# Performance work log

Measured on AMD Instinct MI355X. Metric: run time of the kernel, lower is better.

## Reference

```python
import jax, jax.numpy as jnp
import numpy as np

N_NODES = 100000
N_EDGES = 1600000
IN_FEATS = 128
N_HIDDEN = 128
N_CLASSES = 16
INIT_EPS = 0.0
N_GIN_LAYERS = 4  # n_layers + 1


def setup_inputs() -> dict:
    key = jax.random.key(0)
    ks = jax.random.split(key, 16)
    features = jax.random.normal(ks[0], (N_NODES, IN_FEATS), dtype=jnp.float32)
    src = jax.random.randint(ks[1], (N_EDGES,), 0, N_NODES, dtype=jnp.int64)
    dst = jax.random.randint(ks[2], (N_EDGES,), 0, N_NODES, dtype=jnp.int64)
    def linear(k, fin, fout):
        bound = 1.0 / np.sqrt(fin)
        kw, kb = jax.random.split(k)
        W = jax.random.uniform(kw, (fin, fout), jnp.float32, -bound, bound)
        b = jax.random.uniform(kb, (fout,), jnp.float32, -bound, bound)
        return W, b
    W0, b0 = linear(ks[3], IN_FEATS, N_HIDDEN)
    W1, b1 = linear(ks[4], N_HIDDEN, N_HIDDEN)
    W2, b2 = linear(ks[5], N_HIDDEN, N_HIDDEN)
    W3, b3 = linear(ks[6], N_HIDDEN, N_CLASSES)
    eps = jnp.full((N_GIN_LAYERS,), INIT_EPS, dtype=jnp.float32)
    return {"features": features, "src": src, "dst": dst,
            "W0": W0, "b0": b0, "W1": W1, "b1": b1,
            "W2": W2, "b2": b2, "W3": W3, "b3": b3, "eps": eps}


def _mean_agg(h, src, dst, inv_deg):
    # gather neighbor features along edges, sum into dst, divide by in-degree
    agg = jax.ops.segment_sum(h[src], dst, num_segments=N_NODES)
    return agg * inv_deg


def _gin_layer(h, src, dst, inv_deg, eps, W, b, relu):
    z = (1.0 + eps) * h + _mean_agg(h, src, dst, inv_deg)
    out = z @ W + b  # Dropout is identity in eval mode
    return jax.nn.relu(out) if relu else out


def reference(features, src, dst, W0, b0, W1, b1, W2, b2, W3, b3, eps):
    deg = jax.ops.segment_sum(jnp.ones((src.shape[0],), features.dtype), dst,
                              num_segments=N_NODES)
    inv_deg = (1.0 / jnp.maximum(deg, 1.0))[:, None]
    h = _gin_layer(features, src, dst, inv_deg, eps[0], W0, b0, relu=True)
    h = _gin_layer(h, src, dst, inv_deg, eps[1], W1, b1, relu=True)
    h = _gin_layer(h, src, dst, inv_deg, eps[2], W2, b2, relu=True)
    h = _gin_layer(h, src, dst, inv_deg, eps[3], W3, b3, relu=False)
    return h
```

## Files before the change

kernel.cpp:

```cpp
#include <hip/hip_runtime.h>

#define NODES 100000
#define EDGES 1600000
#define FEATS 128
#define NCLS  16

#define BSH    6
#define BNODES 64
#define NB     ((NODES + BNODES - 1) / BNODES)
#define CHUNK  8192
#define NBLK   ((EDGES + CHUNK - 1) / CHUNK)
#define NHIST  (NB * NBLK)
#define BCAP   2048
#define NGRP   ((NODES + 15) / 16)

typedef unsigned int  u32;
typedef unsigned short u16;
typedef unsigned long long u64;
typedef __attribute__((ext_vector_type(8))) short short8;
typedef __attribute__((ext_vector_type(4))) float f32x4;

__device__ __forceinline__ float b2f(u16 v){ return __uint_as_float(((u32)v)<<16); }
__device__ __forceinline__ u16 f2b(float f){
  u32 u = __float_as_uint(f);
  u += 0x7fffu + ((u>>16)&1u);
  return (u16)(u>>16);
}
__device__ __forceinline__ float blo(u32 p){ return __uint_as_float(p<<16); }
__device__ __forceinline__ float bhi(u32 p){ return __uint_as_float(p & 0xffff0000u); }

__device__ __forceinline__ void gload16(const u16* g, u16* l){
  __builtin_amdgcn_global_load_lds(
      (const __attribute__((address_space(1))) u32*)g,
      (__attribute__((address_space(3))) u32*)l, 16, 0, 0);
}


__global__ __launch_bounds__(256) void pA_k(const int* __restrict__ dst,
                                            int* __restrict__ gh, int E){
  __shared__ int hist[NB];
  int t = threadIdx.x, blk = blockIdx.x;
  for (int j = t; j < NB; j += 256) hist[j] = 0;
  __syncthreads();
  int e0 = blk*CHUNK, e1 = e0 + CHUNK; if (e1 > E) e1 = E;
  for (int e = e0 + t; e < e1; e += 256) atomicAdd(&hist[dst[e] >> BSH], 1);
  __syncthreads();
  for (int j = t; j < NB; j += 256) gh[j*NBLK + blk] = hist[j];
}


__global__ __launch_bounds__(256) void scan1_k(const int* __restrict__ in, int* __restrict__ out,
                                               int* __restrict__ bsum, int n){
  __shared__ int sh[256];
  int t = threadIdx.x;
  int base = blockIdx.x*2048 + t*8;
  int v[8]; int s = 0;
  #pragma unroll
  for (int j=0;j<8;++j) v[j] = (base+j < n) ? in[base+j] : 0;
  #pragma unroll
  for (int j=0;j<8;++j){ int tmp = v[j]; v[j] = s; s += tmp; }
  sh[t] = s; __syncthreads();
  for (int off=1; off<256; off<<=1){
    int x = (t>=off) ? sh[t-off] : 0;
    __syncthreads();
    sh[t] += x;
    __syncthreads();
  }
  int excl = sh[t] - s;
  #pragma unroll
  for (int j=0;j<8;++j) if (base+j < n) out[base+j] = excl + v[j];
  if (t == 255) bsum[blockIdx.x] = sh[255];
}

__global__ __launch_bounds__(256) void scan2_k(const int* __restrict__ bsum,
                                               int* __restrict__ boff, int nb){
  __shared__ int sh[256];
  int t = threadIdx.x;
  int v = (t < nb) ? bsum[t] : 0;
  sh[t] = v; __syncthreads();
  for (int off=1; off<256; off<<=1){
    int x = (t>=off) ? sh[t-off] : 0;
    __syncthreads();
    sh[t] += x;
    __syncthreads();
  }
  if (t < nb) boff[t] = sh[t] - v;
}

__global__ void scan3_k(int* __restrict__ gscan, const int* __restrict__ boff,
                        int* __restrict__ bstart, int n){
  int i = blockIdx.x*256 + threadIdx.x;
  if (i < n){
    int v = gscan[i] + boff[i>>11];
    gscan[i] = v;
    if (i % NBLK == 0) bstart[i / NBLK] = v;
    if (i == 0) bstart[NB] = EDGES;
  }
}


__global__ __launch_bounds__(256) void pC_k(const int* __restrict__ src,
    const int* __restrict__ dst, const int* __restrict__ gscan,
    u32* __restrict__ elist, int E){
  __shared__ int A[NB];
  __shared__ int B[NB];
  __shared__ int sp[256];
  __shared__ u32 pay[CHUNK];
  __shared__ u16 bkt[CHUNK];
  int t = threadIdx.x, blk = blockIdx.x;
  for (int j = t; j < NB; j += 256) A[j] = 0;
  __syncthreads();
  int e0 = blk*CHUNK, e1 = e0 + CHUNK; if (e1 > E) e1 = E;
  int cnt = e1 - e0;
  for (int e = e0 + t; e < e1; e += 256) atomicAdd(&A[dst[e] >> BSH], 1);
  __syncthreads();
  {
    int base = t*7;
    int cv[7]; int s = 0;
    #pragma unroll
    for (int j=0;j<7;++j){ int idx = base+j; cv[j] = (idx < NB) ? A[idx] : 0; s += cv[j]; }
    sp[t] = s; __syncthreads();
    for (int off=1; off<256; off<<=1){
      int x = (t>=off) ? sp[t-off] : 0;
      __syncthreads();
      sp[t] += x;
      __syncthreads();
    }
    int run = sp[t] - s;
    #pragma unroll
    for (int j=0;j<7;++j){
      int idx = base+j;
      if (idx < NB){ A[idx] = run; B[idx] = run; run += cv[j]; }
    }
  }
  __syncthreads();
  for (int j = t; j < NB; j += 256) A[j] = gscan[j*NBLK + blk] - A[j];
  __syncthreads();
  for (int e = e0 + t; e < e1; e += 256){
    int d = dst[e];
    int b = d >> BSH;
    u32 w = ((u32)(d & (BNODES-1)) << 17) | (u32)src[e];
    int r = atomicAdd(&B[b], 1);
    pay[r] = w; bkt[r] = (u16)b;
  }
  __syncthreads();
  for (int i = t; i < cnt; i += 256){
    int b = bkt[i];
    elist[i + A[b]] = pay[i];
  }
}


__global__ __launch_bounds__(256) void csr_k(u32* __restrict__ elist,
    const int* __restrict__ bstart, int* __restrict__ offs, int* __restrict__ degs,
    float* __restrict__ invd, int M){
  __shared__ int hist[BNODES];
  __shared__ int pos[BNODES];
  __shared__ u32 buf[BCAP];
  __shared__ u32 buf2[BCAP];
  int b = blockIdx.x, t = threadIdx.x;
  if (b == 0 && t == 0) offs[M] = EDGES;
  if (t < BNODES) hist[t] = 0;
  __syncthreads();
  int s0 = bstart[b];
  int cnt = bstart[b+1] - s0; if (cnt > BCAP) cnt = BCAP;
  u32* el = elist + s0;
  for (int e = t; e < cnt; e += 256){
    u32 w = el[e];
    buf[e] = w;
    atomicAdd(&hist[w>>17], 1);
  }
  __syncthreads();
  if (t < BNODES){
    int v = hist[t];
    int s = v;
    for (int off = 1; off < BNODES; off <<= 1){
      int x = __shfl_up(s, off);
      if (t >= off) s += x;
    }
    int excl = s - v;
    pos[t] = excl;
    int node = b*BNODES + t;
    if (node < M){
      offs[node] = s0 + excl;
      degs[node] = v;
      invd[node] = 1.f / fmaxf((float)v, 1.f);
    }
  }
  __syncthreads();
  for (int e = t; e < cnt; e += 256){
    u32 w = buf[e];
    int p = atomicAdd(&pos[w>>17], 1);
    buf2[p] = w;
  }
  __syncthreads();
  for (int e = t; e < cnt; e += 256) el[e] = buf2[e];
}


__global__ __launch_bounds__(256) void convw4_k(const float* __restrict__ W0,
    const float* __restrict__ W1, const float* __restrict__ W2,
    const float* __restrict__ W3, u16* __restrict__ Wt0, u16* __restrict__ Wt1,
    u16* __restrict__ Wt2, u16* __restrict__ Wt3){
  int i = blockIdx.x*256 + threadIdx.x;
  if (i < 128*128){
    int k = i >> 7, n = i & 127;
    Wt0[n*128 + k] = f2b(W0[i]);
    Wt1[n*128 + k] = f2b(W1[i]);
    Wt2[n*128 + k] = f2b(W2[i]);
  }
  if (i < 128*16){
    int k = i >> 4, n = i & 15;
    Wt3[n*128 + k] = f2b(W3[i]);
  }
}


template<int NT, bool F32>
__global__ __launch_bounds__(256) void gemm_k(const void* __restrict__ hv,
                                              const u16* __restrict__ Wt,
                                              u16* __restrict__ y, int M){
  const int K = FEATS;
  const int N = NT*16;
  __shared__ __align__(128) u16 wbuf[NT*16*128];
  int t = threadIdx.x;
  #pragma unroll
  for (int i=0;i<NT;++i){
    int g16 = i*2048 + t*8;
    int n   = g16 >> 7;
    int cb2 = (g16 & 127) * 2;
    short8 wv = *(const short8*)(Wt + g16);
    *(short8*)((char*)wbuf + n*256 + (cb2 ^ ((n&7)<<4))) = wv;
  }
  __syncthreads();

  int lane = t & 63;
  int wave = t >> 6;
  int m    = lane & 15;
  int quad = lane >> 4;
  int row0 = (blockIdx.x*4 + wave)*16;
  if (row0 >= M) return;
  int rowA = row0 + m; if (rowA > M-1) rowA = M-1;

  f32x4 acc[NT];
  #pragma unroll
  for (int j=0;j<NT;++j) acc[j] = (f32x4){0.f,0.f,0.f,0.f};

  #pragma unroll
  for (int kb=0; kb<4; ++kb){
    short8 a;
    if constexpr (F32){
      const float* pa = (const float*)hv + (size_t)rowA*K + quad*8 + kb*32;
      float4 x0 = ((const float4*)pa)[0];
      float4 x1 = ((const float4*)pa)[1];
      union { u16 u[8]; short8 s; } au;
      au.u[0]=f2b(x0.x); au.u[1]=f2b(x0.y); au.u[2]=f2b(x0.z); au.u[3]=f2b(x0.w);
      au.u[4]=f2b(x1.x); au.u[5]=f2b(x1.y); au.u[6]=f2b(x1.z); au.u[7]=f2b(x1.w);
      a = au.s;
    } else {
      const u16* pa = (const u16*)hv + (size_t)rowA*K + quad*8 + kb*32;
      a = *(const short8*)pa;
    }
    #pragma unroll
    for (int j=0;j<NT;++j){
      short8 b = *(const short8*)((const char*)wbuf + (j*16+m)*256
                                  + ((kb*64 + quad*16) ^ ((m&7)<<4)));
      acc[j] = __builtin_amdgcn_mfma_f32_16x16x32_bf16(a, b, acc[j], 0, 0, 0);
    }
  }

  #pragma unroll
  for (int j=0;j<NT;++j){
    #pragma unroll
    for (int r=0;r<4;++r){
      int row = row0 + quad*4 + r;
      if (row < M) y[(size_t)row*N + j*16 + m] = f2b(acc[j][r]);
    }
  }
}


#define TRRD(dstv, lit) asm volatile("ds_read_b64_tr_b16 %0, %1 offset:" lit \
                                     : "=v"(dstv) : "v"(trb0))

template<int NTO>
__global__ __launch_bounds__(256) void fagg_k(const u16* __restrict__ y,
    const u32* __restrict__ el, const int* __restrict__ offs,
    const float* __restrict__ invd, const float* __restrict__ bias,
    const float* __restrict__ epsv, int ei,
    const u16* __restrict__ Wn,
    u16* __restrict__ yout){
  __shared__ __align__(128) u16 ybuf[4][4096];
  __shared__ __align__(128) u16 wbuf[NTO*16*128];
  int t = threadIdx.x;
  int lane = t & 63;
  int wave = t >> 6;
  int grp = blockIdx.x*4 + wave;
  bool valid = grp < NGRP;

  #pragma unroll
  for (int i=0;i<NTO;++i){
    int g16 = i*2048 + t*8;
    int n   = g16 >> 7;
    int cb2 = (g16 & 127) * 2;
    short8 wv = *(const short8*)(Wn + g16);
    *(short8*)((char*)wbuf + n*256 + (cb2 ^ ((n&7)<<4))) = wv;
  }
  __syncthreads();
  if (!valid) return;

  int v0 = grp << 4;
  int m    = lane & 15;
  int quad = lane >> 4;
  int li   = lane & 31;
  u32 tgt = (u32)(((grp & 3) << 4) + m);

  u16* lb0 = &ybuf[wave][0];
  typedef __attribute__((address_space(3))) u16 lds_u16;
  u32 lbaddr = (u32)(size_t)(lds_u16*)lb0;
  u32 trb0 = lbaddr + (u32)(quad*2048) + (u32)(m*8);

  int rsel = (lane & 7) >> 1;
  int gcol = ((lane >> 3) << 4) + ((lane & 1) << 3);

  int e0 = offs[v0];
  int e1 = offs[v0 + 16];
  int nstep = (e1 - e0 + 31) >> 5;

  f32x4 acc[8];
  #pragma unroll
  for (int cb=0;cb<8;++cb) acc[cb] = (f32x4){0.f,0.f,0.f,0.f};

  for (int st = 0; st < nstep; ++st){
    int idx = e0 + (st<<5) + li;
    u32 w = (idx < e1) ? el[idx] : 0xFFFE0000u;

    #pragma unroll
    for (int i=0;i<8;++i){
      u32 ws = (u32)__shfl((int)w, 4*i + rsel);
      int srow = (int)(ws & 0x1FFFFu);
      gload16(y + ((size_t)srow << 7) + gcol, lb0 + i*512);
    }

    union { u32 wv[4]; short8 s; } au;
    #pragma unroll
    for (int p=0;p<4;++p){
      u32 w0 = (u32)__shfl((int)w, quad*8 + 2*p);
      u32 w1 = (u32)__shfl((int)w, quad*8 + 2*p + 1);
      au.wv[p] = (((w0>>17) == tgt) ? 0x3F80u : 0u)
               | (((w1>>17) == tgt) ? 0x3F800000u : 0u);
    }

    asm volatile("s_waitcnt vmcnt(0)" ::: "memory");
    __builtin_amdgcn_sched_barrier(0);

    u64 tt[16];
    TRRD(tt[0],  "0");    TRRD(tt[1],  "1024");
    TRRD(tt[2],  "128");  TRRD(tt[3],  "1152");
    TRRD(tt[4],  "256");  TRRD(tt[5],  "1280");
    TRRD(tt[6],  "384");  TRRD(tt[7],  "1408");
    TRRD(tt[8],  "512");  TRRD(tt[9],  "1536");
    TRRD(tt[10], "640");  TRRD(tt[11], "1664");
    TRRD(tt[12], "768");  TRRD(tt[13], "1792");
    TRRD(tt[14], "896");  TRRD(tt[15], "1920");
    asm volatile("s_waitcnt lgkmcnt(0)" ::: "memory");
    __builtin_amdgcn_sched_barrier(0);

    #pragma unroll
    for (int cb=0;cb<8;++cb){
      union { u64 d[2]; short8 s; } bu;
      bu.d[0] = tt[2*cb]; bu.d[1] = tt[2*cb+1];
      acc[cb] = __builtin_amdgcn_mfma_f32_16x16x32_bf16(au.s, bu.s, acc[cb], 0, 0, 0);
    }
  }

  float myinv = invd[v0 + m];
  float invr[4];
  #pragma unroll
  for (int r=0;r<4;++r) invr[r] = __shfl(myinv, quad*4 + r);
  float e1s = 1.f + epsv[ei];
  u16* zl = lb0;
  #pragma unroll
  for (int cb=0;cb<8;++cb){
    float bi = bias[cb*16 + m];
    #pragma unroll
    for (int r=0;r<4;++r){
      size_t off = (size_t)(v0 + quad*4 + r)*FEATS + cb*16 + m;
      float self = b2f(y[off]);
      float h = fmaxf(e1s*self + invr[r]*acc[cb][r] + bi, 0.f);
      zl[(quad*4 + r)*136 + cb*16 + m] = f2b(h);
    }
  }

  short8 af[4];
  #pragma unroll
  for (int kb=0;kb<4;++kb)
    af[kb] = *(const short8*)(zl + m*136 + kb*32 + quad*8);

  #pragma unroll
  for (int nb=0;nb<NTO;++nb){
    f32x4 a2 = (f32x4){0.f,0.f,0.f,0.f};
    #pragma unroll
    for (int kb=0;kb<4;++kb){
      short8 bf = *(const short8*)((const char*)wbuf + (nb*16+m)*256
                                   + ((kb*64 + quad*16) ^ ((m&7)<<4)));
      a2 = __builtin_amdgcn_mfma_f32_16x16x32_bf16(af[kb], bf, a2, 0, 0, 0);
    }
    #pragma unroll
    for (int r=0;r<4;++r)
      yout[(size_t)(v0 + quad*4 + r)*(NTO*16) + nb*16 + m] = f2b(a2[r]);
  }
}


__global__ __launch_bounds__(256) void aggF2_k(const u16* __restrict__ y,
    const u32* __restrict__ el, const int* __restrict__ offs,
    const int* __restrict__ degs, const float* __restrict__ invd,
    const float* __restrict__ bias, const float* __restrict__ epsv,
    float* __restrict__ out, int M){
  int lane = threadIdx.x & 63;
  int v = blockIdx.x*4 + (threadIdx.x >> 6);
  if (v >= M) return;
  int sub = lane >> 3;
  int f2  = lane & 7;
  const u32* y2 = (const u32*)y;
  int start = offs[v], deg = degs[v];
  float acc0 = 0.f, acc1 = 0.f;
  for (int e = sub; e < deg; e += 8){
    u32 s = el[start + e] & 0x1FFFFu;
    u32 p = y2[(size_t)s*8 + f2];
    acc0 += blo(p); acc1 += bhi(p);
  }
  acc0 += __shfl_xor(acc0, 8);  acc1 += __shfl_xor(acc1, 8);
  acc0 += __shfl_xor(acc0, 16); acc1 += __shfl_xor(acc1, 16);
  acc0 += __shfl_xor(acc0, 32); acc1 += __shfl_xor(acc1, 32);
  if (sub == 0){
    u32 pv = y2[(size_t)v*8 + f2];
    float2 bi = ((const float2*)bias)[f2];
    float e1s = 1.f + epsv[3];
    float inv = invd[v];
    out[(size_t)v*NCLS + 2*f2    ] = e1s*blo(pv) + inv*acc0 + bi.x;
    out[(size_t)v*NCLS + 2*f2 + 1] = e1s*bhi(pv) + inv*acc1 + bi.y;
  }
}


extern "C" void kernel_launch(void* const* d_in, const int* in_sizes, int n_in,
                              void* d_out, int out_size, void* d_ws, size_t ws_size,
                              hipStream_t stream){
  const float* feats = (const float*)d_in[0];
  const int*   src   = (const int*)d_in[1];
  const int*   dst   = (const int*)d_in[2];
  const float* W0 = (const float*)d_in[3];  const float* b0 = (const float*)d_in[4];
  const float* W1 = (const float*)d_in[5];  const float* b1 = (const float*)d_in[6];
  const float* W2 = (const float*)d_in[7];  const float* b2 = (const float*)d_in[8];
  const float* W3 = (const float*)d_in[9];  const float* b3 = (const float*)d_in[10];
  const float* eps = (const float*)d_in[11];

  char* w = (char*)d_ws;
  auto alloc = [&](size_t bytes)->char*{
    char* p = w; w += (bytes + 255) & ~(size_t)255; return p;
  };
  int*  gh    = (int*)alloc(sizeof(int)*NHIST);
  int*  gscan = (int*)alloc(sizeof(int)*NHIST);
  int*  bsum  = (int*)alloc(sizeof(int)*256);
  int*  boff  = (int*)alloc(sizeof(int)*256);
  int*  bstart= (int*)alloc(sizeof(int)*(NB+1));
  int*  offs  = (int*)alloc(sizeof(int)*(NODES+1));
  int*  degs  = (int*)alloc(sizeof(int)*NODES);
  float* invd = (float*)alloc(sizeof(float)*NODES);
  u32*  elist = (u32*)alloc(sizeof(u32)*EDGES);
  u16*  hb    = (u16*)alloc(sizeof(u16)*(size_t)NODES*FEATS);
  u16*  yb    = (u16*)alloc(sizeof(u16)*(size_t)NODES*FEATS);
  u16*  Wt0   = (u16*)alloc(sizeof(u16)*128*128);
  u16*  Wt1   = (u16*)alloc(sizeof(u16)*128*128);
  u16*  Wt2   = (u16*)alloc(sizeof(u16)*128*128);
  u16*  Wt3   = (u16*)alloc(sizeof(u16)*16*128);

  pA_k<<<NBLK, 256, 0, stream>>>(dst, gh, EDGES);
  int snb = (NHIST + 2047)/2048;
  scan1_k<<<snb, 256, 0, stream>>>(gh, gscan, bsum, NHIST);
  scan2_k<<<1, 256, 0, stream>>>(bsum, boff, snb);
  scan3_k<<<(NHIST+255)/256, 256, 0, stream>>>(gscan, boff, bstart, NHIST);
  pC_k<<<NBLK, 256, 0, stream>>>(src, dst, gscan, elist, EDGES);
  csr_k<<<NB, 256, 0, stream>>>(elist, bstart, offs, degs, invd, NODES);

  convw4_k<<<(128*128+255)/256, 256, 0, stream>>>(W0, W1, W2, W3, Wt0, Wt1, Wt2, Wt3);

  int gblocks = (NODES + 63)/64;
  int mblocks = (NGRP + 3)/4;
  int ablocks = (NODES + 3)/4;

  gemm_k<8, true><<<gblocks, 256, 0, stream>>>(feats, Wt0, yb, NODES);
  fagg_k<8><<<mblocks, 256, 0, stream>>>(yb, elist, offs, invd, b0, eps, 0, Wt1, hb);
  fagg_k<8><<<mblocks, 256, 0, stream>>>(hb, elist, offs, invd, b1, eps, 1, Wt2, yb);
  fagg_k<1><<<mblocks, 256, 0, stream>>>(yb, elist, offs, invd, b2, eps, 2, Wt3, hb);
  aggF2_k<<<ablocks, 256, 0, stream>>>(hb, elist, offs, degs, invd, b3, eps, (float*)d_out, NODES);
}
```

Before: 412.5 us.

## Double-buffer neighbor gathers and process two node groups per wave in fused aggregation

The fused aggregate+GEMM kernel now gives each wave two 16-node groups, g and g+HNG, and runs their edge steps as one continuous loop. Edge-index loads are prefetched one step ahead, and row gathers go into a double-buffered LDS region, so the next step's global loads overlap the current step's transpose reads and MFMAs. The weight tile is no longer staged in LDS and is read directly from global memory in the per-group epilogue. This removes the block-wide weight preload and barrier, at the cost of uncached-in-LDS weight reads, hand-tuned vmcnt counts that must match the number of outstanding loads, and half as many waves to hide latency.

```diff
diff --git a/kernel.cpp b/kernel.cpp
--- a/kernel.cpp
+++ b/kernel.cpp
@@ -13,6 +13,7 @@
 #define NHIST  (NB * NBLK)
 #define BCAP   2048
 #define NGRP   ((NODES + 15) / 16)
+#define HNG    3125
 
 typedef unsigned int  u32;
 typedef unsigned short u16;
@@ -281,7 +282,7 @@
 
 
 #define TRRD(dstv, lit) asm volatile("ds_read_b64_tr_b16 %0, %1 offset:" lit \
-                                     : "=v"(dstv) : "v"(trb0))
+                                     : "=v"(dstv) : "v"(trb_i))
 
 template<int NTO>
 __global__ __launch_bounds__(256) void fagg_k(const u16* __restrict__ y,
@@ -290,32 +291,20 @@
     const float* __restrict__ epsv, int ei,
     const u16* __restrict__ Wn,
     u16* __restrict__ yout){
-  __shared__ __align__(128) u16 ybuf[4][4096];
-  __shared__ __align__(128) u16 wbuf[NTO*16*128];
+  __shared__ __align__(128) u16 ybuf[4][2][4096];
   int t = threadIdx.x;
   int lane = t & 63;
   int wave = t >> 6;
-  int grp = blockIdx.x*4 + wave;
-  bool valid = grp < NGRP;
-
-  #pragma unroll
-  for (int i=0;i<NTO;++i){
-    int g16 = i*2048 + t*8;
-    int n   = g16 >> 7;
-    int cb2 = (g16 & 127) * 2;
-    short8 wv = *(const short8*)(Wn + g16);
-    *(short8*)((char*)wbuf + n*256 + (cb2 ^ ((n&7)<<4))) = wv;
-  }
-  __syncthreads();
-  if (!valid) return;
-
-  int v0 = grp << 4;
+  int g0 = blockIdx.x*4 + wave;
+  if (g0 >= HNG) return;
+  int g1 = g0 + HNG;
   int m    = lane & 15;
   int quad = lane >> 4;
   int li   = lane & 31;
-  u32 tgt = (u32)(((grp & 3) << 4) + m);
-
-  u16* lb0 = &ybuf[wave][0];
+  u32 tgtA = (u32)(((g0 & 3) << 4) + m);
+  u32 tgtB = (u32)(((g1 & 3) << 4) + m);
+
+  u16* lb0 = &ybuf[wave][0][0];
   typedef __attribute__((address_space(3))) u16 lds_u16;
   u32 lbaddr = (u32)(size_t)(lds_u16*)lb0;
   u32 trb0 = lbaddr + (u32)(quad*2048) + (u32)(m*8);
@@ -323,37 +312,105 @@
   int rsel = (lane & 7) >> 1;
   int gcol = ((lane >> 3) << 4) + ((lane & 1) << 3);
 
-  int e0 = offs[v0];
-  int e1 = offs[v0 + 16];
-  int nstep = (e1 - e0 + 31) >> 5;
+  int e0A = offs[g0 << 4], e1A = offs[(g0 << 4) + 16];
+  int e0B = offs[g1 << 4], e1B = offs[(g1 << 4) + 16];
+  int SA = (e1A - e0A + 31) >> 5; if (SA < 1) SA = 1;
+  int SB = (e1B - e0B + 31) >> 5; if (SB < 1) SB = 1;
+  int S  = SA + SB;
 
   f32x4 acc[8];
   #pragma unroll
   for (int cb=0;cb<8;++cb) acc[cb] = (f32x4){0.f,0.f,0.f,0.f};
 
-  for (int st = 0; st < nstep; ++st){
-    int idx = e0 + (st<<5) + li;
-    u32 w = (idx < e1) ? el[idx] : 0xFFFE0000u;
-
+  auto elp = [&](int st)->const u32*{
+    int idx = (st < SA) ? (e0A + (st<<5) + li) : (e0B + ((st-SA)<<5) + li);
+    if (idx > EDGES-1) idx = EDGES-1;
+    return el + idx;
+  };
+  auto maskw = [&](u32 v, int st)->u32{
+    bool ok;
+    if (st < SA){ ok = (e0A + (st<<5) + li) < e1A; }
+    else        { ok = (st < S) && ((e0B + ((st-SA)<<5) + li) < e1B); }
+    return ok ? v : 0xFFFE0000u;
+  };
+  auto gathers = [&](u32 wm, u16* dstbuf){
     #pragma unroll
     for (int i=0;i<8;++i){
-      u32 ws = (u32)__shfl((int)w, 4*i + rsel);
+      u32 ws = (u32)__shfl((int)wm, 4*i + rsel);
       int srow = (int)(ws & 0x1FFFFu);
-      gload16(y + ((size_t)srow << 7) + gcol, lb0 + i*512);
-    }
-
+      gload16(y + ((size_t)srow << 7) + gcol, dstbuf + i*512);
+    }
+  };
+  float e1s = 1.f + epsv[ei];
+  auto tail = [&](int g, u16* scr, bool mid){
+    int v0 = g << 4;
+    float myinv = invd[v0 + m];
+    float invr[4];
+    #pragma unroll
+    for (int r=0;r<4;++r) invr[r] = __shfl(myinv, quad*4 + r);
+    #pragma unroll
+    for (int cb=0;cb<8;++cb){
+      float bi = bias[cb*16 + m];
+      #pragma unroll
+      for (int r=0;r<4;++r){
+        size_t off = (size_t)(v0 + quad*4 + r)*FEATS + cb*16 + m;
+        float self = b2f(y[off]);
+        float h = fmaxf(e1s*self + invr[r]*acc[cb][r] + bi, 0.f);
+        scr[(quad*4 + r)*136 + cb*16 + m] = f2b(h);
+      }
+    }
+    short8 af[4];
+    #pragma unroll
+    for (int kb=0;kb<4;++kb)
+      af[kb] = *(const short8*)(scr + m*136 + kb*32 + quad*8);
+    #pragma unroll
+    for (int nb=0;nb<NTO;++nb){
+      f32x4 a2 = (f32x4){0.f,0.f,0.f,0.f};
+      #pragma unroll
+      for (int kb=0;kb<4;++kb){
+        short8 bf = *(const short8*)(Wn + (size_t)(nb*16 + m)*FEATS + kb*32 + quad*8);
+        a2 = __builtin_amdgcn_mfma_f32_16x16x32_bf16(af[kb], bf, a2, 0, 0, 0);
+      }
+      #pragma unroll
+      for (int r=0;r<4;++r)
+        yout[(size_t)(v0 + quad*4 + r)*(NTO*16) + nb*16 + m] = f2b(a2[r]);
+    }
+    if (mid){
+      #pragma unroll
+      for (int cb=0;cb<8;++cb) acc[cb] = (f32x4){0.f,0.f,0.f,0.f};
+      asm volatile("s_waitcnt vmcnt(9)" ::: "memory");
+    }
+  };
+
+  u32 v0w;
+  asm volatile("global_load_dword %0, %1, off" : "=v"(v0w) : "v"(elp(0)));
+  asm volatile("s_waitcnt vmcnt(0)" : "+v"(v0w) :: "memory");
+  u32 wcur = maskw(v0w, 0);
+  u32 vnext;
+  asm volatile("global_load_dword %0, %1, off" : "=v"(vnext) : "v"(elp(1)));
+  gathers(wcur, lb0);
+
+  for (int st = 0; st < S; ++st){
+    asm volatile("s_waitcnt vmcnt(8)" : "+v"(vnext) :: "memory");
+    u32 wn = maskw(vnext, st+1);
+    u32 vfut;
+    asm volatile("global_load_dword %0, %1, off" : "=v"(vfut) : "v"(elp(st+2)));
+    gathers(wn, lb0 + (((st+1)&1) << 12));
+
+    u32 tgt = (st < SA) ? tgtA : tgtB;
     union { u32 wv[4]; short8 s; } au;
     #pragma unroll
     for (int p=0;p<4;++p){
-      u32 w0 = (u32)__shfl((int)w, quad*8 + 2*p);
-      u32 w1 = (u32)__shfl((int)w, quad*8 + 2*p + 1);
+      u32 w0 = (u32)__shfl((int)wcur, quad*8 + 2*p);
+      u32 w1 = (u32)__shfl((int)wcur, quad*8 + 2*p + 1);
       au.wv[p] = (((w0>>17) == tgt) ? 0x3F80u : 0u)
                | (((w1>>17) == tgt) ? 0x3F800000u : 0u);
     }
 
-    asm volatile("s_waitcnt vmcnt(0)" ::: "memory");
+    asm volatile("s_waitcnt vmcnt(9)" ::: "memory");
     __builtin_amdgcn_sched_barrier(0);
 
+    u32 trb_i = trb0 + (u32)((st&1) << 13);
     u64 tt[16];
     TRRD(tt[0],  "0");    TRRD(tt[1],  "1024");
     TRRD(tt[2],  "128");  TRRD(tt[3],  "1152");
@@ -372,44 +429,15 @@
       bu.d[0] = tt[2*cb]; bu.d[1] = tt[2*cb+1];
       acc[cb] = __builtin_amdgcn_mfma_f32_16x16x32_bf16(au.s, bu.s, acc[cb], 0, 0, 0);
     }
-  }
-
-  float myinv = invd[v0 + m];
-  float invr[4];
-  #pragma unroll
-  for (int r=0;r<4;++r) invr[r] = __shfl(myinv, quad*4 + r);
-  float e1s = 1.f + epsv[ei];
-  u16* zl = lb0;
-  #pragma unroll
-  for (int cb=0;cb<8;++cb){
-    float bi = bias[cb*16 + m];
-    #pragma unroll
-    for (int r=0;r<4;++r){
-      size_t off = (size_t)(v0 + quad*4 + r)*FEATS + cb*16 + m;
-      float self = b2f(y[off]);
-      float h = fmaxf(e1s*self + invr[r]*acc[cb][r] + bi, 0.f);
-      zl[(quad*4 + r)*136 + cb*16 + m] = f2b(h);
-    }
-  }
-
-  short8 af[4];
-  #pragma unroll
-  for (int kb=0;kb<4;++kb)
-    af[kb] = *(const short8*)(zl + m*136 + kb*32 + quad*8);
-
-  #pragma unroll
-  for (int nb=0;nb<NTO;++nb){
-    f32x4 a2 = (f32x4){0.f,0.f,0.f,0.f};
-    #pragma unroll
-    for (int kb=0;kb<4;++kb){
-      short8 bf = *(const short8*)((const char*)wbuf + (nb*16+m)*256
-                                   + ((kb*64 + quad*16) ^ ((m&7)<<4)));
-      a2 = __builtin_amdgcn_mfma_f32_16x16x32_bf16(af[kb], bf, a2, 0, 0, 0);
-    }
-    #pragma unroll
-    for (int r=0;r<4;++r)
-      yout[(size_t)(v0 + quad*4 + r)*(NTO*16) + nb*16 + m] = f2b(a2[r]);
-  }
+
+    if (st == SA-1){
+      tail(g0, lb0 + ((st&1) << 12), true);
+    }
+
+    wcur = wn; vnext = vfut;
+  }
+  asm volatile("s_waitcnt vmcnt(0)" ::: "memory");
+  tail(g1, lb0 + (((S-1)&1) << 12), false);
 }
 
 
@@ -488,7 +516,7 @@
   convw4_k<<<(128*128+255)/256, 256, 0, stream>>>(W0, W1, W2, W3, Wt0, Wt1, Wt2, Wt3);
 
   int gblocks = (NODES + 63)/64;
-  int mblocks = (NGRP + 3)/4;
+  int mblocks = (HNG + 3)/4;
   int ablocks = (NODES + 3)/4;
 
   gemm_k<8, true><<<gblocks, 256, 0, stream>>>(feats, Wt0, yb, NODES);
```

After: 452.5 us. 1.1x slower.

## Replace two-level bucketed CSR build with global atomic histogram and scatter

Applied to the files above, without the earlier changes.

The CSR construction used a bucketed counting sort: per-chunk histograms over 64-node buckets, a large scan, a block-local scatter and a per-bucket local sort. It becomes a per-node global atomic degree histogram, a scan over nodes, and a direct scatter using global atomics on per-node cursors. This removes the large NHIST scan and the shared-memory staging, at the cost of 3.2M global atomics and scattered writes. Edge order within each node is now nondeterministic, which changes floating-point summation order.

```diff
diff --git a/kernel.cpp b/kernel.cpp
--- a/kernel.cpp
+++ b/kernel.cpp
@@ -4,15 +4,7 @@
 #define EDGES 1600000
 #define FEATS 128
 #define NCLS  16
-
-#define BSH    6
-#define BNODES 64
-#define NB     ((NODES + BNODES - 1) / BNODES)
-#define CHUNK  8192
-#define NBLK   ((EDGES + CHUNK - 1) / CHUNK)
-#define NHIST  (NB * NBLK)
-#define BCAP   2048
-#define NGRP   ((NODES + 15) / 16)
+#define NGRP  ((NODES + 15) / 16)
 
 typedef unsigned int  u32;
 typedef unsigned short u16;
@@ -36,18 +28,16 @@
 }
 
 
-__global__ __launch_bounds__(256) void pA_k(const int* __restrict__ dst,
-                                            int* __restrict__ gh, int E){
-  __shared__ int hist[NB];
-  int t = threadIdx.x, blk = blockIdx.x;
-  for (int j = t; j < NB; j += 256) hist[j] = 0;
-  __syncthreads();
-  int e0 = blk*CHUNK, e1 = e0 + CHUNK; if (e1 > E) e1 = E;
-  for (int e = e0 + t; e < e1; e += 256) atomicAdd(&hist[dst[e] >> BSH], 1);
-  __syncthreads();
-  for (int j = t; j < NB; j += 256) gh[j*NBLK + blk] = hist[j];
-}
-
+__global__ __launch_bounds__(256) void zero_k(int* __restrict__ a, int n){
+  int i = blockIdx.x*256 + threadIdx.x;
+  if (i < n) a[i] = 0;
+}
+
+__global__ __launch_bounds__(256) void hist_k(const int* __restrict__ dst,
+                                              int* __restrict__ degs, int E){
+  int e = blockIdx.x*256 + threadIdx.x;
+  if (e < E) atomicAdd(&degs[dst[e]], 1);
+}
 
 __global__ __launch_bounds__(256) void scan1_k(const int* __restrict__ in, int* __restrict__ out,
                                                int* __restrict__ bsum, int n){
@@ -87,114 +77,26 @@
   if (t < nb) boff[t] = sh[t] - v;
 }
 
-__global__ void scan3_k(int* __restrict__ gscan, const int* __restrict__ boff,
-                        int* __restrict__ bstart, int n){
+__global__ __launch_bounds__(256) void scan3n_k(const int* __restrict__ gscan,
+    const int* __restrict__ boff, const int* __restrict__ degs,
+    int* __restrict__ offs, int* __restrict__ pos, float* __restrict__ invd, int n){
   int i = blockIdx.x*256 + threadIdx.x;
   if (i < n){
     int v = gscan[i] + boff[i>>11];
-    gscan[i] = v;
-    if (i % NBLK == 0) bstart[i / NBLK] = v;
-    if (i == 0) bstart[NB] = EDGES;
-  }
-}
-
-
-__global__ __launch_bounds__(256) void pC_k(const int* __restrict__ src,
-    const int* __restrict__ dst, const int* __restrict__ gscan,
-    u32* __restrict__ elist, int E){
-  __shared__ int A[NB];
-  __shared__ int B[NB];
-  __shared__ int sp[256];
-  __shared__ u32 pay[CHUNK];
-  __shared__ u16 bkt[CHUNK];
-  int t = threadIdx.x, blk = blockIdx.x;
-  for (int j = t; j < NB; j += 256) A[j] = 0;
-  __syncthreads();
-  int e0 = blk*CHUNK, e1 = e0 + CHUNK; if (e1 > E) e1 = E;
-  int cnt = e1 - e0;
-  for (int e = e0 + t; e < e1; e += 256) atomicAdd(&A[dst[e] >> BSH], 1);
-  __syncthreads();
-  {
-    int base = t*7;
-    int cv[7]; int s = 0;
-    #pragma unroll
-    for (int j=0;j<7;++j){ int idx = base+j; cv[j] = (idx < NB) ? A[idx] : 0; s += cv[j]; }
-    sp[t] = s; __syncthreads();
-    for (int off=1; off<256; off<<=1){
-      int x = (t>=off) ? sp[t-off] : 0;
-      __syncthreads();
-      sp[t] += x;
-      __syncthreads();
-    }
-    int run = sp[t] - s;
-    #pragma unroll
-    for (int j=0;j<7;++j){
-      int idx = base+j;
-      if (idx < NB){ A[idx] = run; B[idx] = run; run += cv[j]; }
-    }
-  }
-  __syncthreads();
-  for (int j = t; j < NB; j += 256) A[j] = gscan[j*NBLK + blk] - A[j];
-  __syncthreads();
-  for (int e = e0 + t; e < e1; e += 256){
+    offs[i] = v; pos[i] = v;
+    invd[i] = 1.f / fmaxf((float)degs[i], 1.f);
+    if (i == 0) offs[n] = EDGES;
+  }
+}
+
+__global__ __launch_bounds__(256) void scat_k(const int* __restrict__ src,
+    const int* __restrict__ dst, int* __restrict__ pos, u32* __restrict__ elist, int E){
+  int e = blockIdx.x*256 + threadIdx.x;
+  if (e < E){
     int d = dst[e];
-    int b = d >> BSH;
-    u32 w = ((u32)(d & (BNODES-1)) << 17) | (u32)src[e];
-    int r = atomicAdd(&B[b], 1);
-    pay[r] = w; bkt[r] = (u16)b;
-  }
-  __syncthreads();
-  for (int i = t; i < cnt; i += 256){
-    int b = bkt[i];
-    elist[i + A[b]] = pay[i];
-  }
-}
-
-
-__global__ __launch_bounds__(256) void csr_k(u32* __restrict__ elist,
-    const int* __restrict__ bstart, int* __restrict__ offs, int* __restrict__ degs,
-    float* __restrict__ invd, int M){
-  __shared__ int hist[BNODES];
-  __shared__ int pos[BNODES];
-  __shared__ u32 buf[BCAP];
-  __shared__ u32 buf2[BCAP];
-  int b = blockIdx.x, t = threadIdx.x;
-  if (b == 0 && t == 0) offs[M] = EDGES;
-  if (t < BNODES) hist[t] = 0;
-  __syncthreads();
-  int s0 = bstart[b];
-  int cnt = bstart[b+1] - s0; if (cnt > BCAP) cnt = BCAP;
-  u32* el = elist + s0;
-  for (int e = t; e < cnt; e += 256){
-    u32 w = el[e];
-    buf[e] = w;
-    atomicAdd(&hist[w>>17], 1);
-  }
-  __syncthreads();
-  if (t < BNODES){
-    int v = hist[t];
-    int s = v;
-    for (int off = 1; off < BNODES; off <<= 1){
-      int x = __shfl_up(s, off);
-      if (t >= off) s += x;
-    }
-    int excl = s - v;
-    pos[t] = excl;
-    int node = b*BNODES + t;
-    if (node < M){
-      offs[node] = s0 + excl;
-      degs[node] = v;
-      invd[node] = 1.f / fmaxf((float)v, 1.f);
-    }
-  }
-  __syncthreads();
-  for (int e = t; e < cnt; e += 256){
-    u32 w = buf[e];
-    int p = atomicAdd(&pos[w>>17], 1);
-    buf2[p] = w;
-  }
-  __syncthreads();
-  for (int e = t; e < cnt; e += 256) el[e] = buf2[e];
+    int p = atomicAdd(&pos[d], 1);
+    elist[p] = ((u32)(d & 63) << 17) | (u32)src[e];
+  }
 }
 
 
@@ -461,13 +363,12 @@
   auto alloc = [&](size_t bytes)->char*{
     char* p = w; w += (bytes + 255) & ~(size_t)255; return p;
   };
-  int*  gh    = (int*)alloc(sizeof(int)*NHIST);
-  int*  gscan = (int*)alloc(sizeof(int)*NHIST);
+  int*  degs  = (int*)alloc(sizeof(int)*NODES);
+  int*  gscan = (int*)alloc(sizeof(int)*NODES);
   int*  bsum  = (int*)alloc(sizeof(int)*256);
   int*  boff  = (int*)alloc(sizeof(int)*256);
-  int*  bstart= (int*)alloc(sizeof(int)*(NB+1));
   int*  offs  = (int*)alloc(sizeof(int)*(NODES+1));
-  int*  degs  = (int*)alloc(sizeof(int)*NODES);
+  int*  pos   = (int*)alloc(sizeof(int)*NODES);
   float* invd = (float*)alloc(sizeof(float)*NODES);
   u32*  elist = (u32*)alloc(sizeof(u32)*EDGES);
   u16*  hb    = (u16*)alloc(sizeof(u16)*(size_t)NODES*FEATS);
@@ -477,13 +378,16 @@
   u16*  Wt2   = (u16*)alloc(sizeof(u16)*128*128);
   u16*  Wt3   = (u16*)alloc(sizeof(u16)*16*128);
 
-  pA_k<<<NBLK, 256, 0, stream>>>(dst, gh, EDGES);
-  int snb = (NHIST + 2047)/2048;
-  scan1_k<<<snb, 256, 0, stream>>>(gh, gscan, bsum, NHIST);
+  int eblocks = (EDGES + 255)/256;
+  int nblocks = (NODES + 255)/256;
+  int snb     = (NODES + 2047)/2048;
+
+  zero_k<<<nblocks, 256, 0, stream>>>(degs, NODES);
+  hist_k<<<eblocks, 256, 0, stream>>>(dst, degs, EDGES);
+  scan1_k<<<snb, 256, 0, stream>>>(degs, gscan, bsum, NODES);
   scan2_k<<<1, 256, 0, stream>>>(bsum, boff, snb);
-  scan3_k<<<(NHIST+255)/256, 256, 0, stream>>>(gscan, boff, bstart, NHIST);
-  pC_k<<<NBLK, 256, 0, stream>>>(src, dst, gscan, elist, EDGES);
-  csr_k<<<NB, 256, 0, stream>>>(elist, bstart, offs, degs, invd, NODES);
+  scan3n_k<<<nblocks, 256, 0, stream>>>(gscan, boff, degs, offs, pos, invd, NODES);
+  scat_k<<<eblocks, 256, 0, stream>>>(src, dst, pos, elist, EDGES);
 
   convw4_k<<<(128*128+255)/256, 256, 0, stream>>>(W0, W1, W2, W3, Wt0, Wt1, Wt2, Wt3);
 
```

New measurement: 551.1 us. 1.34x slower.
